# Kernel tuning notes

Hardware: AMD Instinct MI355X
Metric: run time of the kernel (lower is better)

The kernel has to match this reference:

```python
import jax, jax.numpy as jnp
import numpy as np

K = 5          # number of neighbors (topk k=5+1, drop self)
EPS = 1e-05    # hparams['epsilon'] for gentropy term


def setup_inputs() -> dict:
    key = jax.random.key(0)
    k1, k2, k3, k4, k5 = jax.random.split(key, 5)
    B, D, C, N = 256, 256, 64, 200000
    features = jax.random.normal(k1, (B, D), dtype=jnp.float32)
    W = jax.random.normal(k2, (D, C), dtype=jnp.float32) * 0.05
    b = jnp.zeros((C,), dtype=jnp.float32)
    fea_bank = jax.random.normal(k3, (N, D), dtype=jnp.float32)
    # score bank holds softmax outputs -> make rows valid probability distributions
    score_bank = jax.nn.softmax(jax.random.normal(k4, (N, C), dtype=jnp.float32), axis=-1)
    trg_idx = jax.random.randint(k5, (B,), 0, N, dtype=jnp.int64)
    return {"features": features, "W": W, "b": b,
            "fea_bank": fea_bank, "score_bank": score_bank, "trg_idx": trg_idx}


def reference(features, W, b, fea_bank, score_bank, trg_idx):
    sg = jax.lax.stop_gradient
    B = features.shape[0]
    C = W.shape[1]

    logits = features @ W + b                       # classifier(features)
    softmax_out = jax.nn.softmax(logits, axis=-1)   # [B, C] (differentiable)

    # --- everything bank-related is under torch.no_grad in the original ---
    nrm = jnp.maximum(jnp.linalg.norm(features, axis=1, keepdims=True), 1e-12)
    f_norm = sg(features / nrm)                     # F.normalize(features)
    fb = sg(fea_bank.at[trg_idx].set(f_norm))        # fea_bank[trg_idx] = f_norm
    sb = sg(score_bank.at[trg_idx].set(sg(softmax_out)))

    dist = f_norm @ fb.T                             # [B, N]
    _, idx_near = jax.lax.top_k(dist, K + 1)
    idx_near = idx_near[:, 1:]                       # [B, K] drop self

    score_near = sb[idx_near]                        # [B, K, C]
    fea_near = fb[idx_near]                          # [B, K, D]

    dist2 = jnp.einsum('bkd,nd->bkn', fea_near, fb)  # [B, K, N]
    _, idx_nn = jax.lax.top_k(dist2, K + 1)
    idx_nn = idx_nn[:, :, 1:]                        # [B, K, K]

    match = (idx_nn == trg_idx[:, None, None]).sum(-1).astype(jnp.float32)  # [B, K]
    weight = jnp.where(match > 0.0, match, jnp.float32(0.1))                # [B, K]
    weight_kk = jnp.full((B, K * K), 0.1, dtype=jnp.float32)  # fill_(0.1) overwrites

    score_near_kk = sb[idx_nn].reshape(B, K * K, C)  # [B, K*K, C]
    # --- end no_grad region ---

    # F.kl_div(input, target, reduction='none') = target * (log(target) - input)
    # (original passes probabilities, not log-probs, as input -- kept faithfully)
    kl_kk = score_near_kk * (jnp.log(score_near_kk) - softmax_out[:, None, :])
    loss = jnp.mean((kl_kk.sum(-1) * weight_kk).sum(1))

    kl_n = score_near * (jnp.log(score_near) - softmax_out[:, None, :])
    loss = loss + jnp.mean((kl_n.sum(-1) * weight).sum(1))

    msoftmax = softmax_out.mean(axis=0)
    gentropy = jnp.sum(msoftmax * jnp.log(msoftmax + EPS))
    loss = loss + gentropy
    return loss
```

## Files before the change

### kernel.cpp

```cpp
#include <hip/hip_runtime.h>
#include <hip/hip_bf16.h>
#include <math.h>

#define B_SZ   256
#define D_DIM  256
#define C_DIM  64
#define N_CAND 200000
#define K_TOP  5
#define CH32   32
#define CH32_SH 8192
#define QTILE_SH 16384
#define NCH32  (N_CAND / CH32)
#define CMSTR  6256
#define NCHJ1  16
#define NCHJ2  32
#define S1     ((NCH32 + NCHJ1 - 1) / NCHJ1)
#define S2     ((NCH32 + NCHJ2 - 1) / NCHJ2)
#define MAXC   192

typedef short bf16x8 __attribute__((ext_vector_type(8)));
typedef float f32x16 __attribute__((ext_vector_type(16)));
typedef unsigned short u16x8 __attribute__((ext_vector_type(8)));

__device__ __forceinline__ bool better(float v1, int i1, float v2, int i2) {
    return (v1 > v2) || (v1 == v2 && i1 < i2);
}

__device__ __forceinline__ void insert6f(float* lv, int* li, float v, int idx) {
    if (better(v, idx, lv[5], li[5])) {
        lv[5] = v; li[5] = idx;
        #pragma unroll
        for (int k = 5; k > 0; --k) {
            if (better(lv[k], li[k], lv[k - 1], li[k - 1])) {
                float tv = lv[k]; lv[k] = lv[k - 1]; lv[k - 1] = tv;
                int   ti = li[k]; li[k] = li[k - 1]; li[k - 1] = ti;
            }
        }
    }
}

__device__ __forceinline__ void merge6(const float* av, const int* ai,
                                       const float* bv, const int* bi,
                                       float* ov, int* oi) {
    int ia = 0, ib = 0;
    #pragma unroll
    for (int k = 0; k < 6; ++k) {
        bool ta;
        if (ia >= 6)      ta = false;
        else if (ib >= 6) ta = true;
        else              ta = better(av[ia], ai[ia], bv[ib], bi[ib]);
        if (ta) { ov[k] = av[ia]; oi[k] = ai[ia]; ++ia; }
        else    { ov[k] = bv[ib]; oi[k] = bi[ib]; ++ib; }
    }
}

__device__ __forceinline__ unsigned short bf16rne(float x) {
    unsigned int u = __float_as_uint(x);
    unsigned int r = u + 0x7fffu + ((u >> 16) & 1u);
    return (unsigned short)(r >> 16);
}

__device__ __forceinline__ float bf16f(unsigned short h) {
    return __uint_as_float(((unsigned)h) << 16);
}

__device__ __forceinline__ u16x8 pack8(float4 a, float4 b) {
    u16x8 h;
    h[0] = bf16rne(a.x); h[1] = bf16rne(a.y); h[2] = bf16rne(a.z); h[3] = bf16rne(a.w);
    h[4] = bf16rne(b.x); h[5] = bf16rne(b.y); h[6] = bf16rne(b.z); h[7] = bf16rne(b.w);
    return h;
}

__global__ void k_init(int* pos_of, float* accp) {
    int i = blockIdx.x * 256 + threadIdx.x;
    if (i < N_CAND) pos_of[i] = -1;
    if (i == 0) accp[0] = 0.f;
}

__global__ void k_scatter(const int* __restrict__ trg, int* __restrict__ pos_of) {
    int j = threadIdx.x;
    atomicMax(&pos_of[trg[j]], j);
}

__global__ __launch_bounds__(256) void k_prep(const float* __restrict__ features,
                                              const float* __restrict__ W,
                                              const float* __restrict__ bias,
                                              float* __restrict__ f_norm,
                                              float* __restrict__ softm) {
    int b = blockIdx.x, t = threadIdx.x;
    __shared__ float row[256];
    __shared__ float red[256];
    float x = features[b * D_DIM + t];
    row[t] = x; red[t] = x * x;
    __syncthreads();
    for (int s = 128; s > 0; s >>= 1) {
        if (t < s) red[t] += red[t + s];
        __syncthreads();
    }
    float nrm = fmaxf(sqrtf(red[0]), 1e-12f);
    f_norm[b * D_DIM + t] = x / nrm;
    if (t < C_DIM) {
        float acc = bias[t];
        for (int d = 0; d < D_DIM; ++d) acc = fmaf(row[d], W[d * C_DIM + t], acc);
        float mx = acc;
        for (int off = 32; off > 0; off >>= 1) mx = fmaxf(mx, __shfl_xor(mx, off, 64));
        float e = expf(acc - mx);
        float ssum = e;
        for (int off = 32; off > 0; off >>= 1) ssum += __shfl_xor(ssum, off, 64);
        softm[b * C_DIM + t] = e / ssum;
    }
}

__global__ __launch_bounds__(256) void k_convert(const float* __restrict__ fea_bank,
                                                 const float* __restrict__ f_norm,
                                                 const int* __restrict__ pos_of,
                                                 short* __restrict__ bank) {
    int cc = blockIdx.x, t = threadIdx.x;
    int r = t >> 2, q4 = t & 3;
    int n = cc * 64 + r;
    int p = pos_of[n];
    const float* src = (p >= 0) ? (f_norm + (size_t)p * D_DIM)
                                : (fea_bank + (size_t)n * D_DIM);
    short* dst = bank + (size_t)(cc * 2 + (r >> 5)) * CH32_SH;
    int rl = r & 31;
    #pragma unroll
    for (int i = 0; i < 8; ++i) {
        int kk = i * 32 + q4 * 8;
        float4 a = *(const float4*)(src + kk);
        float4 b = *(const float4*)(src + kk + 4);
        int e = ((kk >> 4) * 64) + (((kk >> 3) & 1) * 32) + rl;
        *(u16x8*)(dst + (size_t)e * 8) = pack8(a, b);
    }
}

__global__ __launch_bounds__(256) void k_permq(const float* __restrict__ rows,
                                               const float* __restrict__ fea_bank,
                                               const int* __restrict__ idx,
                                               const int* __restrict__ pos_of,
                                               short* __restrict__ dst,
                                               unsigned short* __restrict__ qplain) {
    int tile = blockIdx.x, t = threadIdx.x;
    int r = t >> 2, q4 = t & 3;
    const float* src;
    if (idx) {
        int n = idx[tile * 64 + r];
        int p = pos_of[n];
        src = (p >= 0) ? (rows + (size_t)p * D_DIM) : (fea_bank + (size_t)n * D_DIM);
    } else {
        src = rows + (size_t)(tile * 64 + r) * D_DIM;
    }
    short* d = dst + (size_t)tile * QTILE_SH;
    unsigned short* qp = qplain + (size_t)(tile * 64 + r) * D_DIM;
    #pragma unroll
    for (int i = 0; i < 8; ++i) {
        int kk = i * 32 + q4 * 8;
        float4 a = *(const float4*)(src + kk);
        float4 b = *(const float4*)(src + kk + 4);
        u16x8 h = pack8(a, b);
        int e = ((kk >> 4) * 128) + ((r >> 5) * 64) + (((kk >> 3) & 1) * 32) + (r & 31);
        *(u16x8*)(d + (size_t)e * 8) = h;
        *(u16x8*)(qp + kk) = h;
    }
}

__global__ __launch_bounds__(256, 2) void dist_max(const short* __restrict__ qbf,
                                                   const short* __restrict__ bank,
                                                   unsigned short* __restrict__ cmax,
                                                   int nqt, int swz,
                                                   int S, int nchj) {
    __shared__ __align__(16) short sbuf[4 * CH32_SH];
    __shared__ unsigned short cmaxbuf[32 * 256];

    int slab, qt;
    if (swz) {
        int bid = blockIdx.x;
        int xcd = bid & 7;
        int rem = bid >> 3;
        qt = rem % nqt;
        slab = (rem / nqt) * 8 + xcd;
        if (slab >= S) return;
    } else {
        slab = blockIdx.x;
        qt = blockIdx.y;
    }
    const int cfirst = slab * nchj;
    int nch = NCH32 - cfirst; if (nch > nchj) nch = nchj;

    const int t   = threadIdx.x;
    const int w   = t >> 6;
    const int l   = t & 63;
    const int khv = l >> 5;
    const int col = l & 31;

    const short* qtile = qbf + (size_t)(qt * 4 + w) * QTILE_SH;
    bf16x8 bfr0[16], bfr1[16];
    #pragma unroll
    for (int ks = 0; ks < 16; ++ks) {
        bfr0[ks] = *(const bf16x8*)(qtile + (size_t)(ks * 128      + l) * 8);
        bfr1[ks] = *(const bf16x8*)(qtile + (size_t)(ks * 128 + 64 + l) * 8);
    }
    #pragma unroll
    for (int ks = 0; ks < 16; ++ks)
        asm volatile("" : "+v"(bfr0[ks]), "+v"(bfr1[ks]));

    const short* sbase = bank + (size_t)cfirst * CH32_SH;

    #pragma unroll
    for (int c = 0; c < 3; ++c) {
        const short* g = sbase + (size_t)c * CH32_SH;
        short* lbase = sbuf + (size_t)c * CH32_SH;
        #pragma unroll
        for (int i = 0; i < 4; ++i) {
            const short* gp = g + (size_t)(i * 256 + t) * 8;
            short* lp = lbase + (size_t)(i * 256 + w * 64) * 8;
            __builtin_amdgcn_global_load_lds(
                (const __attribute__((address_space(1))) void*)gp,
                (__attribute__((address_space(3))) void*)lp, 16, 0, 0);
        }
    }

    for (int ch = 0; ch < nch; ++ch) {
        int ahead = nch - 1 - ch;
        if (ahead >= 2)      asm volatile("s_waitcnt vmcnt(8)" ::: "memory");
        else if (ahead == 1) asm volatile("s_waitcnt vmcnt(4)" ::: "memory");
        else                 asm volatile("s_waitcnt vmcnt(0)" ::: "memory");
        __builtin_amdgcn_s_barrier();
        __builtin_amdgcn_sched_barrier(0);

        const short* cb = sbuf + (size_t)(ch & 3) * CH32_SH;

        f32x16 a0 = {}, a1 = {};
        __builtin_amdgcn_s_setprio(1);
        #pragma unroll
        for (int ks = 0; ks < 16; ++ks) {
            bf16x8 fa = *(const bf16x8*)(cb + (size_t)(ks * 64 + l) * 8);
            a0 = __builtin_amdgcn_mfma_f32_32x32x16_bf16(fa, bfr0[ks], a0, 0, 0, 0);
            a1 = __builtin_amdgcn_mfma_f32_32x32x16_bf16(fa, bfr1[ks], a1, 0, 0, 0);
        }
        __builtin_amdgcn_s_setprio(0);

        float m0 = a0[0], m1 = a1[0];
        #pragma unroll
        for (int r = 1; r < 16; ++r) { m0 = fmaxf(m0, a0[r]); m1 = fmaxf(m1, a1[r]); }
        m0 = fmaxf(m0, __shfl_xor(m0, 32, 64));
        m1 = fmaxf(m1, __shfl_xor(m1, 32, 64));
        if (khv == 0) {
            cmaxbuf[ch * 256 + w * 64 + col]      = bf16rne(m0);
            cmaxbuf[ch * 256 + w * 64 + 32 + col] = bf16rne(m1);
        }

        if (ch + 3 < nch) {
            const short* g = sbase + (size_t)(ch + 3) * CH32_SH;
            short* lbase = sbuf + (size_t)((ch + 3) & 3) * CH32_SH;
            #pragma unroll
            for (int i = 0; i < 4; ++i) {
                const short* gp = g + (size_t)(i * 256 + t) * 8;
                short* lp = lbase + (size_t)(i * 256 + w * 64) * 8;
                __builtin_amdgcn_global_load_lds(
                    (const __attribute__((address_space(1))) void*)gp,
                    (__attribute__((address_space(3))) void*)lp, 16, 0, 0);
            }
        }
    }

    __syncthreads();
    {
        size_t gbase = (size_t)(qt * 256 + t) * CMSTR + cfirst;
        int c0 = 0;
        for (; c0 + 8 <= nch; c0 += 8) {
            u16x8 h;
            #pragma unroll
            for (int i = 0; i < 8; ++i) h[i] = cmaxbuf[(c0 + i) * 256 + t];
            *(u16x8*)(cmax + gbase + c0) = h;
        }
        for (; c0 < nch; ++c0) cmax[gbase + c0] = cmaxbuf[c0 * 256 + t];
        int cend = CMSTR - cfirst; if (cend > nchj) cend = nchj;
        for (int cp = nch; cp < cend; ++cp) cmax[gbase + cp] = 0xFF7F;
    }
}

__global__ __launch_bounds__(256) void k_select(const unsigned short* __restrict__ cmax,
                                                const unsigned short* __restrict__ qplain,
                                                const short* __restrict__ bank,
                                                int* __restrict__ out_idx) {
    int q = blockIdx.x, t = threadIdx.x;
    __shared__ float sv[256][6];
    __shared__ int   si[256][6];
    __shared__ float qrow[256];
    __shared__ int cnt;
    __shared__ int list[MAXC];

    const unsigned short* row = cmax + (size_t)q * CMSTR;

    float lv[6]; int li[6];
    #pragma unroll
    for (int k = 0; k < 6; ++k) { lv[k] = -3.4e38f; li[k] = 0x7fffffff; }
    for (int c0 = t * 8; c0 < CMSTR; c0 += 2048) {
        u16x8 h = *(const u16x8*)(row + c0);
        float m8 = bf16f(h[0]);
        #pragma unroll
        for (int i = 1; i < 8; ++i) m8 = fmaxf(m8, bf16f(h[i]));
        if (better(m8, c0, lv[5], li[5])) {
            #pragma unroll
            for (int i = 0; i < 8; ++i) {
                int c = c0 + i;
                if (c < NCH32) insert6f(lv, li, bf16f(h[i]), c);
            }
        }
    }
    #pragma unroll
    for (int k = 0; k < 6; ++k) { sv[t][k] = lv[k]; si[t][k] = li[k]; }
    if (t == 0) cnt = 0;
    __syncthreads();
    for (int w = 128; w >= 1; w >>= 1) {
        if (t < w) {
            float ov[6]; int oi[6];
            merge6(sv[t], si[t], sv[t + w], si[t + w], ov, oi);
            #pragma unroll
            for (int k = 0; k < 6; ++k) { sv[t][k] = ov[k]; si[t][k] = oi[k]; }
        }
        __syncthreads();
    }
    float tauM = sv[0][5] - 6e-3f;
    __syncthreads();

    for (int c0 = t * 8; c0 < CMSTR; c0 += 2048) {
        u16x8 h = *(const u16x8*)(row + c0);
        float m8 = bf16f(h[0]);
        #pragma unroll
        for (int i = 1; i < 8; ++i) m8 = fmaxf(m8, bf16f(h[i]));
        if (m8 >= tauM) {
            #pragma unroll
            for (int i = 0; i < 8; ++i) {
                int c = c0 + i;
                if (c < NCH32 && bf16f(h[i]) >= tauM) {
                    int k = atomicAdd(&cnt, 1);
                    if (k < MAXC) list[k] = c;
                }
            }
        }
    }
    qrow[t] = bf16f(qplain[(size_t)q * D_DIM + t]);
    __syncthreads();
    int nc = cnt < MAXC ? cnt : MAXC;

    float bv[6]; int bi[6];
    #pragma unroll
    for (int k = 0; k < 6; ++k) { bv[k] = -3.4e38f; bi[k] = 0x7fffffff; }
    const int cand = t >> 3, j = t & 7;
    for (int ci = 0; ci < nc; ++ci) {
        int c = list[ci];
        const short* cb = bank + (size_t)c * CH32_SH;
        u16x8 h0 = *(const u16x8*)(cb + (size_t)(128 * j +  0 + cand) * 8);
        u16x8 h1 = *(const u16x8*)(cb + (size_t)(128 * j + 32 + cand) * 8);
        u16x8 h2 = *(const u16x8*)(cb + (size_t)(128 * j + 64 + cand) * 8);
        u16x8 h3 = *(const u16x8*)(cb + (size_t)(128 * j + 96 + cand) * 8);
        int d0 = j * 32;
        float acc = 0.f;
        #pragma unroll
        for (int d = 0; d < 8; ++d) {
            acc = fmaf(bf16f(h0[d]), qrow[d0 + d], acc);
            acc = fmaf(bf16f(h1[d]), qrow[d0 + 8 + d], acc);
            acc = fmaf(bf16f(h2[d]), qrow[d0 + 16 + d], acc);
            acc = fmaf(bf16f(h3[d]), qrow[d0 + 24 + d], acc);
        }
        acc += __shfl_down(acc, 4, 8);
        acc += __shfl_down(acc, 2, 8);
        acc += __shfl_down(acc, 1, 8);
        if (j == 0) insert6f(bv, bi, acc, c * CH32 + cand);
    }

    #pragma unroll
    for (int k = 0; k < 6; ++k) { sv[t][k] = bv[k]; si[t][k] = bi[k]; }
    __syncthreads();
    for (int w = 128; w >= 1; w >>= 1) {
        if (t < w) {
            float ov[6]; int oi[6];
            merge6(sv[t], si[t], sv[t + w], si[t + w], ov, oi);
            #pragma unroll
            for (int k = 0; k < 6; ++k) { sv[t][k] = ov[k]; si[t][k] = oi[k]; }
        }
        __syncthreads();
    }
    if (t == 0) {
        for (int k = 1; k < 6; ++k) out_idx[q * K_TOP + k - 1] = si[0][k];
    }
}

__global__ void k_loss(const float* __restrict__ softm, const float* __restrict__ score_bank,
                       const int* __restrict__ pos_of, const int* __restrict__ idx_near,
                       const int* __restrict__ idx_nn, const int* __restrict__ trg,
                       float* accp) {
    int b = blockIdx.x, c = threadIdx.x;
    float p_bc = softm[b * C_DIM + c];
    float part = 0.f;
    for (int k = 0; k < K_TOP; ++k) {
        for (int j = 0; j < K_TOP; ++j) {
            int n = idx_nn[(b * K_TOP + k) * K_TOP + j];
            int p = pos_of[n];
            const float* srow = (p >= 0) ? (softm + (size_t)p * C_DIM)
                                         : (score_bank + (size_t)n * C_DIM);
            float s = srow[c];
            float v = s * (logf(s) - p_bc);
            for (int off = 32; off > 0; off >>= 1) v += __shfl_down(v, off, 64);
            if (c == 0) part += 0.1f * v;
        }
    }
    for (int k = 0; k < K_TOP; ++k) {
        int n = idx_near[b * K_TOP + k];
        int p = pos_of[n];
        const float* srow = (p >= 0) ? (softm + (size_t)p * C_DIM)
                                     : (score_bank + (size_t)n * C_DIM);
        float s = srow[c];
        float v = s * (logf(s) - p_bc);
        for (int off = 32; off > 0; off >>= 1) v += __shfl_down(v, off, 64);
        if (c == 0) {
            int m = 0;
            for (int j = 0; j < K_TOP; ++j)
                m += (idx_nn[(b * K_TOP + k) * K_TOP + j] == trg[b]) ? 1 : 0;
            float w = (m > 0) ? (float)m : 0.1f;
            part += w * v;
        }
    }
    if (c == 0) atomicAdd(accp, part * (1.0f / (float)B_SZ));
}

__global__ void k_final(const float* __restrict__ softm, const float* __restrict__ accp,
                        float* __restrict__ out) {
    int c = threadIdx.x;
    float m = 0.f;
    for (int b = 0; b < B_SZ; ++b) m += softm[b * C_DIM + c];
    m *= (1.0f / (float)B_SZ);
    float g = m * logf(m + 1e-5f);
    for (int off = 32; off > 0; off >>= 1) g += __shfl_down(g, off, 64);
    if (c == 0) out[0] = accp[0] + g;
}

extern "C" void kernel_launch(void* const* d_in, const int* in_sizes, int n_in,
                              void* d_out, int out_size, void* d_ws, size_t ws_size,
                              hipStream_t stream) {
    const float* features   = (const float*)d_in[0];
    const float* W          = (const float*)d_in[1];
    const float* bias       = (const float*)d_in[2];
    const float* fea_bank   = (const float*)d_in[3];
    const float* score_bank = (const float*)d_in[4];
    const int*   trg        = (const int*)d_in[5];
    float* out = (float*)d_out;

    char* ws = (char*)d_ws;
    size_t off = 0;
    auto alloc = [&](size_t bytes) -> void* {
        void* p = ws + off;
        off = (off + bytes + 255) & ~(size_t)255;
        return p;
    };
    short* bankbf   = (short*)alloc((size_t)NCH32 * CH32_SH * 2);
    short* q1bf     = (short*)alloc((size_t)(B_SZ / 64) * QTILE_SH * 2);
    short* q2bf     = (short*)alloc((size_t)(B_SZ * K_TOP / 64) * QTILE_SH * 2);
    unsigned short* qplain1 = (unsigned short*)alloc((size_t)B_SZ * D_DIM * 2);
    unsigned short* qplain2 = (unsigned short*)alloc((size_t)B_SZ * K_TOP * D_DIM * 2);
    float* f_norm   = (float*)alloc((size_t)B_SZ * D_DIM * 4);
    float* softm    = (float*)alloc((size_t)B_SZ * C_DIM * 4);
    int*   pos_of   = (int*)alloc((size_t)N_CAND * 4);
    float* accp     = (float*)alloc(4);
    int*   idx_near = (int*)alloc((size_t)B_SZ * K_TOP * 4);
    int*   idx_nn   = (int*)alloc((size_t)B_SZ * K_TOP * K_TOP * 4);
    unsigned short* cmax1 = (unsigned short*)alloc((size_t)B_SZ * CMSTR * 2);
    unsigned short* cmax2 = (unsigned short*)alloc((size_t)B_SZ * K_TOP * CMSTR * 2);

    k_init<<<dim3((N_CAND + 255) / 256), dim3(256), 0, stream>>>(pos_of, accp);
    k_scatter<<<dim3(1), dim3(256), 0, stream>>>(trg, pos_of);
    k_prep<<<dim3(B_SZ), dim3(256), 0, stream>>>(features, W, bias, f_norm, softm);

    k_convert<<<dim3(NCH32 / 2), dim3(256), 0, stream>>>(fea_bank, f_norm, pos_of, bankbf);
    k_permq<<<dim3(B_SZ / 64), dim3(256), 0, stream>>>(
        f_norm, fea_bank, nullptr, pos_of, q1bf, qplain1);

    dist_max<<<dim3(S1, 1), dim3(256), 0, stream>>>(
        q1bf, bankbf, cmax1, 1, 0, S1, NCHJ1);
    k_select<<<dim3(B_SZ), dim3(256), 0, stream>>>(cmax1, qplain1, bankbf, idx_near);

    k_permq<<<dim3(B_SZ * K_TOP / 64), dim3(256), 0, stream>>>(
        f_norm, fea_bank, idx_near, pos_of, q2bf, qplain2);

    {
        int nqt = (B_SZ * K_TOP) / 256;
        int nsg = (S2 + 7) / 8;
        dist_max<<<dim3(nsg * 8 * nqt), dim3(256), 0, stream>>>(
            q2bf, bankbf, cmax2, nqt, 1, S2, NCHJ2);
    }
    k_select<<<dim3(B_SZ * K_TOP), dim3(256), 0, stream>>>(cmax2, qplain2, bankbf, idx_nn);

    k_loss<<<dim3(B_SZ), dim3(64), 0, stream>>>(softm, score_bank, pos_of, idx_near, idx_nn, trg, accp);
    k_final<<<dim3(1), dim3(64), 0, stream>>>(softm, accp, out);
}
```

Baseline: 317.2 us.

## Widen dist_max to 8-wave blocks sharing each bank chunk across more query tiles

```diff
diff --git a/kernel.cpp b/kernel.cpp
--- a/kernel.cpp
+++ b/kernel.cpp
@@ -12,8 +12,8 @@
 #define QTILE_SH 16384
 #define NCH32  (N_CAND / CH32)
 #define CMSTR  6256
-#define NCHJ1  16
-#define NCHJ2  32
+#define NCHJ1  25
+#define NCHJ2  74
 #define S1     ((NCH32 + NCHJ1 - 1) / NCHJ1)
 #define S2     ((NCH32 + NCHJ2 - 1) / NCHJ2)
 #define MAXC   192
@@ -163,13 +163,13 @@
     }
 }
 
-__global__ __launch_bounds__(256, 2) void dist_max(const short* __restrict__ qbf,
+__global__ __launch_bounds__(512, 2) void dist_max(const short* __restrict__ qbf,
                                                    const short* __restrict__ bank,
                                                    unsigned short* __restrict__ cmax,
                                                    int nqt, int swz,
-                                                   int S, int nchj) {
-    __shared__ __align__(16) short sbuf[4 * CH32_SH];
-    __shared__ unsigned short cmaxbuf[32 * 256];
+                                                   int S, int nchj, int maxtile) {
+    __shared__ __align__(16) short sbuf[3 * CH32_SH];
+    __shared__ unsigned short cmaxbuf[8 * 512];
 
     int slab, qt;
     if (swz) {
@@ -192,7 +192,8 @@
     const int khv = l >> 5;
     const int col = l & 31;
 
-    const short* qtile = qbf + (size_t)(qt * 4 + w) * QTILE_SH;
+    int ti = qt * 8 + w; if (ti > maxtile) ti = maxtile;
+    const short* qtile = qbf + (size_t)ti * QTILE_SH;
     bf16x8 bfr0[16], bfr1[16];
     #pragma unroll
     for (int ks = 0; ks < 16; ++ks) {
@@ -200,19 +201,21 @@
         bfr1[ks] = *(const bf16x8*)(qtile + (size_t)(ks * 128 + 64 + l) * 8);
     }
     #pragma unroll
-    for (int ks = 0; ks < 16; ++ks)
-        asm volatile("" : "+v"(bfr0[ks]), "+v"(bfr1[ks]));
+    for (int ks = 0; ks < 16; ++ks) {
+        asm volatile("s_nop 0" : "+v"(bfr0[ks]));
+        asm volatile("s_nop 0" : "+v"(bfr1[ks]));
+    }
 
     const short* sbase = bank + (size_t)cfirst * CH32_SH;
 
     #pragma unroll
-    for (int c = 0; c < 3; ++c) {
+    for (int c = 0; c < 2; ++c) {
         const short* g = sbase + (size_t)c * CH32_SH;
         short* lbase = sbuf + (size_t)c * CH32_SH;
         #pragma unroll
-        for (int i = 0; i < 4; ++i) {
-            const short* gp = g + (size_t)(i * 256 + t) * 8;
-            short* lp = lbase + (size_t)(i * 256 + w * 64) * 8;
+        for (int i = 0; i < 2; ++i) {
+            const short* gp = g + (size_t)(i * 512 + t) * 8;
+            short* lp = lbase + (size_t)(i * 512 + w * 64) * 8;
             __builtin_amdgcn_global_load_lds(
                 (const __attribute__((address_space(1))) void*)gp,
                 (__attribute__((address_space(3))) void*)lp, 16, 0, 0);
@@ -221,13 +224,13 @@
 
     for (int ch = 0; ch < nch; ++ch) {
         int ahead = nch - 1 - ch;
-        if (ahead >= 2)      asm volatile("s_waitcnt vmcnt(8)" ::: "memory");
-        else if (ahead == 1) asm volatile("s_waitcnt vmcnt(4)" ::: "memory");
+        if (ahead >= 2)      asm volatile("s_waitcnt vmcnt(4)" ::: "memory");
+        else if (ahead == 1) asm volatile("s_waitcnt vmcnt(2)" ::: "memory");
         else                 asm volatile("s_waitcnt vmcnt(0)" ::: "memory");
         __builtin_amdgcn_s_barrier();
         __builtin_amdgcn_sched_barrier(0);
 
-        const short* cb = sbuf + (size_t)(ch & 3) * CH32_SH;
+        const short* cb = sbuf + (size_t)(ch % 3) * CH32_SH;
 
         f32x16 a0 = {}, a1 = {};
         __builtin_amdgcn_s_setprio(1);
@@ -245,37 +248,46 @@
         m0 = fmaxf(m0, __shfl_xor(m0, 32, 64));
         m1 = fmaxf(m1, __shfl_xor(m1, 32, 64));
         if (khv == 0) {
-            cmaxbuf[ch * 256 + w * 64 + col]      = bf16rne(m0);
-            cmaxbuf[ch * 256 + w * 64 + 32 + col] = bf16rne(m1);
-        }
-
-        if (ch + 3 < nch) {
-            const short* g = sbase + (size_t)(ch + 3) * CH32_SH;
-            short* lbase = sbuf + (size_t)((ch + 3) & 3) * CH32_SH;
+            cmaxbuf[(ch & 7) * 512 + w * 64 + col]      = bf16rne(m0);
+            cmaxbuf[(ch & 7) * 512 + w * 64 + 32 + col] = bf16rne(m1);
+        }
+
+        if (ch + 2 < nch) {
+            const short* g = sbase + (size_t)(ch + 2) * CH32_SH;
+            short* lbase = sbuf + (size_t)((ch + 2) % 3) * CH32_SH;
             #pragma unroll
-            for (int i = 0; i < 4; ++i) {
-                const short* gp = g + (size_t)(i * 256 + t) * 8;
-                short* lp = lbase + (size_t)(i * 256 + w * 64) * 8;
+            for (int i = 0; i < 2; ++i) {
+                const short* gp = g + (size_t)(i * 512 + t) * 8;
+                short* lp = lbase + (size_t)(i * 512 + w * 64) * 8;
                 __builtin_amdgcn_global_load_lds(
                     (const __attribute__((address_space(1))) void*)gp,
                     (__attribute__((address_space(3))) void*)lp, 16, 0, 0);
             }
         }
-    }
-
-    __syncthreads();
-    {
-        size_t gbase = (size_t)(qt * 256 + t) * CMSTR + cfirst;
-        int c0 = 0;
-        for (; c0 + 8 <= nch; c0 += 8) {
-            u16x8 h;
-            #pragma unroll
-            for (int i = 0; i < 8; ++i) h[i] = cmaxbuf[(c0 + i) * 256 + t];
-            *(u16x8*)(cmax + gbase + c0) = h;
-        }
-        for (; c0 < nch; ++c0) cmax[gbase + c0] = cmaxbuf[c0 * 256 + t];
-        int cend = CMSTR - cfirst; if (cend > nchj) cend = nchj;
-        for (int cp = nch; cp < cend; ++cp) cmax[gbase + cp] = 0xFF7F;
+
+        if ((ch & 7) == 7 || ch == nch - 1) {
+            asm volatile("s_waitcnt lgkmcnt(0)" ::: "memory");
+            __builtin_amdgcn_s_barrier();
+            int chbase = ch & ~7;
+            int cnt = ch - chbase + 1;
+            int tig = qt * 8 + (t >> 6); if (tig > maxtile) tig = maxtile;
+            int gq = tig * 64 + (t & 63);
+            size_t gbase = (size_t)gq * CMSTR + cfirst + chbase;
+            if (cnt == 8) {
+                u16x8 h;
+                #pragma unroll
+                for (int i = 0; i < 8; ++i) h[i] = cmaxbuf[i * 512 + t];
+                *(u16x8*)(cmax + gbase) = h;
+            } else {
+                for (int k = 0; k < cnt; ++k) cmax[gbase + k] = cmaxbuf[k * 512 + t];
+            }
+            if (ch == nch - 1) {
+                int cend = (cfirst + nchj >= NCH32) ? (CMSTR - cfirst) : nchj;
+                for (int cp = nch; cp < cend; ++cp)
+                    cmax[(size_t)gq * CMSTR + cfirst + cp] = 0xFF7F;
+            }
+            __builtin_amdgcn_s_barrier();
+        }
     }
 }
 
@@ -476,18 +488,18 @@
     k_permq<<<dim3(B_SZ / 64), dim3(256), 0, stream>>>(
         f_norm, fea_bank, nullptr, pos_of, q1bf, qplain1);
 
-    dist_max<<<dim3(S1, 1), dim3(256), 0, stream>>>(
-        q1bf, bankbf, cmax1, 1, 0, S1, NCHJ1);
+    dist_max<<<dim3(S1, 1), dim3(512), 0, stream>>>(
+        q1bf, bankbf, cmax1, 1, 0, S1, NCHJ1, 3);
     k_select<<<dim3(B_SZ), dim3(256), 0, stream>>>(cmax1, qplain1, bankbf, idx_near);
 
     k_permq<<<dim3(B_SZ * K_TOP / 64), dim3(256), 0, stream>>>(
         f_norm, fea_bank, idx_near, pos_of, q2bf, qplain2);
 
     {
-        int nqt = (B_SZ * K_TOP) / 256;
+        int nqt = 3;
         int nsg = (S2 + 7) / 8;
-        dist_max<<<dim3(nsg * 8 * nqt), dim3(256), 0, stream>>>(
-            q2bf, bankbf, cmax2, nqt, 1, S2, NCHJ2);
+        dist_max<<<dim3(nsg * 8 * nqt), dim3(512), 0, stream>>>(
+            q2bf, bankbf, cmax2, nqt, 1, S2, NCHJ2, 19);
     }
     k_select<<<dim3(B_SZ * K_TOP), dim3(256), 0, stream>>>(cmax2, qplain2, bankbf, idx_nn);
 
```

New measurement: 443.0 us. +39.6%, slower.
